# Kernel optimization log

Measured on AMD Instinct MI355X. Metric: run time of the kernel, lower is better.

## Reference

```python
import jax, jax.numpy as jnp
import numpy as np

BETA = 0.99
EPS_V = 1e-3
LOG_2PI = float(np.log(2.0 * np.pi))


def setup_inputs() -> dict:
    key = jax.random.key(0)
    ks = jax.random.split(key, 8)
    B, D, H, OUT = 2_097_152, 2, 64, 4  # OUT = 2*2*k (mu + log-var), k=1
    x = jax.random.normal(ks[0], (B, D), dtype=jnp.float32)
    y = jax.random.normal(ks[1], (B, 1, 2), dtype=jnp.float32)
    eps = jax.random.normal(ks[2], (B, 1, 2), dtype=jnp.float32)  # rsample noise
    # small init scale keeps exp(var-head) numerically tame, as trained nets would be
    W1 = 0.5 * jax.random.normal(ks[3], (D, H), dtype=jnp.float32)
    b1 = jnp.zeros((H,), dtype=jnp.float32)
    W2 = 0.1 * jax.random.normal(ks[4], (H, OUT), dtype=jnp.float32)
    b2 = jnp.zeros((OUT,), dtype=jnp.float32)
    Wv = jax.random.normal(ks[5], (D, D), dtype=jnp.float32)
    return {"x": x, "y": y, "eps": eps, "W1": W1, "b1": b1, "W2": W2, "b2": b2, "Wv": Wv}


def _V(z, Wv):
    # positive-definite Lyapunov surrogate: ||z Wv||^2 + eps, keepdims on last axis
    return jnp.sum(jnp.square(z @ Wv), axis=-1, keepdims=True) + EPS_V


def reference(x, y, eps, W1, b1, W2, b2, Wv):
    # fhat: 2 -> 64 -> 4 MLP
    fhatx = jax.nn.relu(x @ W1 + b1) @ W2 + b2            # [B, 4]
    mu = fhatx[..., :2].reshape(-1, 1, 2)                  # [B, 1, 2]
    var = jnp.exp(fhatx[..., 2:]).reshape(-1, 1, 2)        # [B, 1, 2]
    Vx = _V(x, Wv).reshape(-1, 1, 1)                       # [B, 1, 1]
    Vmu = _V(mu, Wv)                                       # [B, 1, 1]
    scale = (BETA * Vx - jax.nn.relu(BETA * Vx - Vmu)) / Vmu
    mu_stable = mu * scale                                 # [B, 1, 2]
    # diagonal-Gaussian rsample (equivalent to MVN with diag_embed(var))
    fx = mu_stable + jnp.sqrt(var) * eps                   # [B, 1, 2]
    # closed-form diagonal MVN log_prob, event dim = 2
    diff = y - mu_stable
    logp = -0.5 * (jnp.sum(diff * diff / var + jnp.log(var), axis=-1) + 2.0 * LOG_2PI)  # [B, 1]
    logp_y = -jnp.sum(logp)
    return fx, logp_y
```

## Files before the change

### kernel.cpp

```cpp
#include <hip/hip_runtime.h>
#include <math.h>


typedef float v2f __attribute__((ext_vector_type(2)));

#define GRID 1024
#define BLOCK 256
#define NPAIR 4
#define LOG_2PI 1.8378770664093453f

__device__ __forceinline__ float rcp_fast(float v) { return __builtin_amdgcn_rcpf(v); }
__device__ __forceinline__ v2f splat(float s) { v2f r; r.x = s; r.y = s; return r; }

__launch_bounds__(BLOCK, 4)
__global__ void mdn_kernel(const float* __restrict__ x,
                           const float* __restrict__ y,
                           const float* __restrict__ eps,
                           const float* __restrict__ W1,
                           const float* __restrict__ b1,
                           const float* __restrict__ W2,
                           const float* __restrict__ b2,
                           const float* __restrict__ Wv,
                           float* __restrict__ fx_out,
                           float* __restrict__ block_part,
                           int n_pairs)
{
    __shared__ float s_part[BLOCK / 64];

    const int t = threadIdx.x;
    const int T = GRID * BLOCK;
    const int g = blockIdx.x * BLOCK + t;

    const float b2_0 = b2[0], b2_1 = b2[1], b2_2 = b2[2], b2_3 = b2[3];
    const float wv00 = Wv[0], wv01 = Wv[1], wv10 = Wv[2], wv11 = Wv[3];

    float4 yv[NPAIR], ev[NPAIR];
    v2f X0[NPAIR], X1[NPAIR];
    v2f A0[NPAIR], A1[NPAIR], A2[NPAIR], A3[NPAIR];

    #pragma unroll
    for (int p = 0; p < NPAIR; ++p) {
        const int rp = g + p * T;
        float4 xv = make_float4(0.f, 0.f, 0.f, 0.f);
        yv[p] = make_float4(0.f, 0.f, 0.f, 0.f);
        ev[p] = make_float4(0.f, 0.f, 0.f, 0.f);
        if (rp < n_pairs) {
            xv    = reinterpret_cast<const float4*>(x)[rp];
            yv[p] = reinterpret_cast<const float4*>(y)[rp];
            ev[p] = reinterpret_cast<const float4*>(eps)[rp];
        }
        X0[p].x = xv.x; X0[p].y = xv.z;
        X1[p].x = xv.y; X1[p].y = xv.w;
        A0[p] = splat(b2_0); A1[p] = splat(b2_1);
        A2[p] = splat(b2_2); A3[p] = splat(b2_3);
    }

    #pragma unroll 2
    for (int c = 0; c < 16; ++c) {
        const float4 wa = *reinterpret_cast<const float4*>(W1 + 4 * c);
        const float4 wb = *reinterpret_cast<const float4*>(W1 + 64 + 4 * c);
        const float4 bb = *reinterpret_cast<const float4*>(b1 + 4 * c);
        const float4 w2r[4] = {
            reinterpret_cast<const float4*>(W2)[4 * c + 0],
            reinterpret_cast<const float4*>(W2)[4 * c + 1],
            reinterpret_cast<const float4*>(W2)[4 * c + 2],
            reinterpret_cast<const float4*>(W2)[4 * c + 3],
        };
        #pragma unroll
        for (int j = 0; j < 4; ++j) {
            const v2f waj = splat((&wa.x)[j]);
            const v2f wbj = splat((&wb.x)[j]);
            const v2f bj  = splat((&bb.x)[j]);
            const v2f w20 = splat(w2r[j].x);
            const v2f w21 = splat(w2r[j].y);
            const v2f w22 = splat(w2r[j].z);
            const v2f w23 = splat(w2r[j].w);
            #pragma unroll
            for (int p = 0; p < NPAIR; ++p) {
                v2f h = __builtin_elementwise_fma(X1[p], wbj, bj);
                h = __builtin_elementwise_fma(X0[p], waj, h);
                h = __builtin_elementwise_max(h, splat(0.f));
                A0[p] = __builtin_elementwise_fma(h, w20, A0[p]);
                A1[p] = __builtin_elementwise_fma(h, w21, A1[p]);
                A2[p] = __builtin_elementwise_fma(h, w22, A2[p]);
                A3[p] = __builtin_elementwise_fma(h, w23, A3[p]);
            }
        }
    }

    float lsum = 0.f;
    #pragma unroll
    for (int p = 0; p < NPAIR; ++p) {
        const int rp = g + p * T;
        float4 fxv;
        #pragma unroll
        for (int hh = 0; hh < 2; ++hh) {
            const float mu0 = hh ? A0[p].y : A0[p].x;
            const float mu1 = hh ? A1[p].y : A1[p].x;
            const float lv0 = hh ? A2[p].y : A2[p].x;
            const float lv1 = hh ? A3[p].y : A3[p].x;
            const float xx0 = hh ? X0[p].y : X0[p].x;
            const float xx1 = hh ? X1[p].y : X1[p].x;
            const float y0 = hh ? yv[p].z : yv[p].x;
            const float y1 = hh ? yv[p].w : yv[p].y;
            const float e0 = hh ? ev[p].z : ev[p].x;
            const float e1 = hh ? ev[p].w : ev[p].y;
            const float zx0 = fmaf(xx0, wv00, xx1 * wv10);
            const float zx1 = fmaf(xx0, wv01, xx1 * wv11);
            const float Vx  = fmaf(zx0, zx0, fmaf(zx1, zx1, 1e-3f));
            const float zm0 = fmaf(mu0, wv00, mu1 * wv10);
            const float zm1 = fmaf(mu0, wv01, mu1 * wv11);
            const float Vmu = fmaf(zm0, zm0, fmaf(zm1, zm1, 1e-3f));
            const float scale = fminf(0.99f * Vx, Vmu) * rcp_fast(Vmu);
            const float ms0 = mu0 * scale, ms1 = mu1 * scale;
            const float f0 = fmaf(__expf(0.5f * lv0), e0, ms0);
            const float f1 = fmaf(__expf(0.5f * lv1), e1, ms1);
            if (hh) { fxv.z = f0; fxv.w = f1; }
            else    { fxv.x = f0; fxv.y = f1; }
            const float d0 = y0 - ms0;
            const float d1 = y1 - ms1;
            const float q = fmaf(d0 * d0, __expf(-lv0), d1 * d1 * __expf(-lv1));
            lsum += fmaf(0.5f, q + lv0 + lv1, LOG_2PI);
        }
        if (rp < n_pairs) reinterpret_cast<float4*>(fx_out)[rp] = fxv;
    }

    #pragma unroll
    for (int off = 32; off; off >>= 1) lsum += __shfl_xor(lsum, off, 64);
    if ((t & 63) == 0) s_part[t >> 6] = lsum;
    __syncthreads();
    if (t == 0) {
        float bs = 0.f;
        #pragma unroll
        for (int w = 0; w < BLOCK / 64; ++w) bs += s_part[w];
        block_part[blockIdx.x] = bs;
    }
}

__launch_bounds__(BLOCK, 1)
__global__ void mdn_reduce_kernel(const float* __restrict__ block_part,
                                  float* __restrict__ logp_out)
{
    __shared__ float s_part[BLOCK / 64];
    const int t = threadIdx.x;
    float s = 0.f;
    #pragma unroll
    for (int k = 0; k < GRID / BLOCK; ++k) s += block_part[t + k * BLOCK];
    #pragma unroll
    for (int off = 32; off; off >>= 1) s += __shfl_xor(s, off, 64);
    if ((t & 63) == 0) s_part[t >> 6] = s;
    __syncthreads();
    if (t == 0) {
        float bs = 0.f;
        #pragma unroll
        for (int w = 0; w < BLOCK / 64; ++w) bs += s_part[w];
        *logp_out = bs;
    }
}

extern "C" void kernel_launch(void* const* d_in, const int* in_sizes, int n_in,
                              void* d_out, int out_size, void* d_ws, size_t ws_size,
                              hipStream_t stream) {
    const float* x   = (const float*)d_in[0];
    const float* y   = (const float*)d_in[1];
    const float* eps = (const float*)d_in[2];
    const float* W1  = (const float*)d_in[3];
    const float* b1  = (const float*)d_in[4];
    const float* W2  = (const float*)d_in[5];
    const float* b2  = (const float*)d_in[6];
    const float* Wv  = (const float*)d_in[7];

    const int B = in_sizes[0] / 2;
    const int n_pairs = B / 2;
    float* fx_out     = (float*)d_out;
    float* logp_out   = fx_out + (size_t)2 * B;
    float* block_part = (float*)d_ws;

    mdn_kernel<<<GRID, BLOCK, 0, stream>>>(x, y, eps, W1, b1, W2, b2, Wv,
                                           fx_out, block_part, n_pairs);
    mdn_reduce_kernel<<<1, BLOCK, 0, stream>>>(block_part, logp_out);
}
```

Baseline: 121.1 us.

## Defer y/eps loads into MLP loop and vectorize epilogue with packed math

```diff
diff --git a/kernel.cpp b/kernel.cpp
--- a/kernel.cpp
+++ b/kernel.cpp
@@ -11,6 +11,45 @@
 
 __device__ __forceinline__ float rcp_fast(float v) { return __builtin_amdgcn_rcpf(v); }
 __device__ __forceinline__ v2f splat(float s) { v2f r; r.x = s; r.y = s; return r; }
+
+__device__ __forceinline__ void mlp_chunk(int c,
+                                          const float* __restrict__ W1,
+                                          const float* __restrict__ b1,
+                                          const float* __restrict__ W2,
+                                          const v2f (&X0)[NPAIR], const v2f (&X1)[NPAIR],
+                                          v2f (&A0)[NPAIR], v2f (&A1)[NPAIR],
+                                          v2f (&A2)[NPAIR], v2f (&A3)[NPAIR])
+{
+    const float4 wa = *reinterpret_cast<const float4*>(W1 + 4 * c);
+    const float4 wb = *reinterpret_cast<const float4*>(W1 + 64 + 4 * c);
+    const float4 bb = *reinterpret_cast<const float4*>(b1 + 4 * c);
+    const float4 w2r[4] = {
+        reinterpret_cast<const float4*>(W2)[4 * c + 0],
+        reinterpret_cast<const float4*>(W2)[4 * c + 1],
+        reinterpret_cast<const float4*>(W2)[4 * c + 2],
+        reinterpret_cast<const float4*>(W2)[4 * c + 3],
+    };
+    #pragma unroll
+    for (int j = 0; j < 4; ++j) {
+        const v2f waj = splat((&wa.x)[j]);
+        const v2f wbj = splat((&wb.x)[j]);
+        const v2f bj  = splat((&bb.x)[j]);
+        const v2f w20 = splat(w2r[j].x);
+        const v2f w21 = splat(w2r[j].y);
+        const v2f w22 = splat(w2r[j].z);
+        const v2f w23 = splat(w2r[j].w);
+        #pragma unroll
+        for (int p = 0; p < NPAIR; ++p) {
+            v2f h = __builtin_elementwise_fma(X1[p], wbj, bj);
+            h = __builtin_elementwise_fma(X0[p], waj, h);
+            h = __builtin_elementwise_max(h, splat(0.f));
+            A0[p] = __builtin_elementwise_fma(h, w20, A0[p]);
+            A1[p] = __builtin_elementwise_fma(h, w21, A1[p]);
+            A2[p] = __builtin_elementwise_fma(h, w22, A2[p]);
+            A3[p] = __builtin_elementwise_fma(h, w23, A3[p]);
+        }
+    }
+}
 
 __launch_bounds__(BLOCK, 4)
 __global__ void mdn_kernel(const float* __restrict__ x,
@@ -34,100 +73,88 @@
     const float b2_0 = b2[0], b2_1 = b2[1], b2_2 = b2[2], b2_3 = b2[3];
     const float wv00 = Wv[0], wv01 = Wv[1], wv10 = Wv[2], wv11 = Wv[3];
 
-    float4 yv[NPAIR], ev[NPAIR];
-    v2f X0[NPAIR], X1[NPAIR];
+    v2f X0[NPAIR], X1[NPAIR], Vx[NPAIR];
     v2f A0[NPAIR], A1[NPAIR], A2[NPAIR], A3[NPAIR];
 
     #pragma unroll
     for (int p = 0; p < NPAIR; ++p) {
         const int rp = g + p * T;
         float4 xv = make_float4(0.f, 0.f, 0.f, 0.f);
-        yv[p] = make_float4(0.f, 0.f, 0.f, 0.f);
-        ev[p] = make_float4(0.f, 0.f, 0.f, 0.f);
-        if (rp < n_pairs) {
-            xv    = reinterpret_cast<const float4*>(x)[rp];
-            yv[p] = reinterpret_cast<const float4*>(y)[rp];
-            ev[p] = reinterpret_cast<const float4*>(eps)[rp];
-        }
+        if (rp < n_pairs) xv = reinterpret_cast<const float4*>(x)[rp];
         X0[p].x = xv.x; X0[p].y = xv.z;
         X1[p].x = xv.y; X1[p].y = xv.w;
         A0[p] = splat(b2_0); A1[p] = splat(b2_1);
         A2[p] = splat(b2_2); A3[p] = splat(b2_3);
     }
+    #pragma unroll
+    for (int p = 0; p < NPAIR; ++p) {
+        const v2f zx0 = __builtin_elementwise_fma(X0[p], splat(wv00), X1[p] * splat(wv10));
+        const v2f zx1 = __builtin_elementwise_fma(X0[p], splat(wv01), X1[p] * splat(wv11));
+        Vx[p] = __builtin_elementwise_fma(zx0, zx0,
+                __builtin_elementwise_fma(zx1, zx1, splat(1e-3f)));
+    }
 
     #pragma unroll 2
-    for (int c = 0; c < 16; ++c) {
-        const float4 wa = *reinterpret_cast<const float4*>(W1 + 4 * c);
-        const float4 wb = *reinterpret_cast<const float4*>(W1 + 64 + 4 * c);
-        const float4 bb = *reinterpret_cast<const float4*>(b1 + 4 * c);
-        const float4 w2r[4] = {
-            reinterpret_cast<const float4*>(W2)[4 * c + 0],
-            reinterpret_cast<const float4*>(W2)[4 * c + 1],
-            reinterpret_cast<const float4*>(W2)[4 * c + 2],
-            reinterpret_cast<const float4*>(W2)[4 * c + 3],
-        };
-        #pragma unroll
-        for (int j = 0; j < 4; ++j) {
-            const v2f waj = splat((&wa.x)[j]);
-            const v2f wbj = splat((&wb.x)[j]);
-            const v2f bj  = splat((&bb.x)[j]);
-            const v2f w20 = splat(w2r[j].x);
-            const v2f w21 = splat(w2r[j].y);
-            const v2f w22 = splat(w2r[j].z);
-            const v2f w23 = splat(w2r[j].w);
-            #pragma unroll
-            for (int p = 0; p < NPAIR; ++p) {
-                v2f h = __builtin_elementwise_fma(X1[p], wbj, bj);
-                h = __builtin_elementwise_fma(X0[p], waj, h);
-                h = __builtin_elementwise_max(h, splat(0.f));
-                A0[p] = __builtin_elementwise_fma(h, w20, A0[p]);
-                A1[p] = __builtin_elementwise_fma(h, w21, A1[p]);
-                A2[p] = __builtin_elementwise_fma(h, w22, A2[p]);
-                A3[p] = __builtin_elementwise_fma(h, w23, A3[p]);
-            }
+    for (int c = 0; c < 12; ++c)
+        mlp_chunk(c, W1, b1, W2, X0, X1, A0, A1, A2, A3);
+
+    float4 yv[NPAIR], ev[NPAIR];
+    #pragma unroll
+    for (int p = 0; p < NPAIR; ++p) {
+        const int rp = g + p * T;
+        yv[p] = make_float4(0.f, 0.f, 0.f, 0.f);
+        ev[p] = make_float4(0.f, 0.f, 0.f, 0.f);
+        if (rp < n_pairs) {
+            yv[p] = reinterpret_cast<const float4*>(y)[rp];
+            ev[p] = reinterpret_cast<const float4*>(eps)[rp];
         }
     }
 
-    float lsum = 0.f;
+    #pragma unroll 2
+    for (int c = 12; c < 16; ++c)
+        mlp_chunk(c, W1, b1, W2, X0, X1, A0, A1, A2, A3);
+
+    v2f lsum = splat(0.f);
     #pragma unroll
     for (int p = 0; p < NPAIR; ++p) {
         const int rp = g + p * T;
-        float4 fxv;
-        #pragma unroll
-        for (int hh = 0; hh < 2; ++hh) {
-            const float mu0 = hh ? A0[p].y : A0[p].x;
-            const float mu1 = hh ? A1[p].y : A1[p].x;
-            const float lv0 = hh ? A2[p].y : A2[p].x;
-            const float lv1 = hh ? A3[p].y : A3[p].x;
-            const float xx0 = hh ? X0[p].y : X0[p].x;
-            const float xx1 = hh ? X1[p].y : X1[p].x;
-            const float y0 = hh ? yv[p].z : yv[p].x;
-            const float y1 = hh ? yv[p].w : yv[p].y;
-            const float e0 = hh ? ev[p].z : ev[p].x;
-            const float e1 = hh ? ev[p].w : ev[p].y;
-            const float zx0 = fmaf(xx0, wv00, xx1 * wv10);
-            const float zx1 = fmaf(xx0, wv01, xx1 * wv11);
-            const float Vx  = fmaf(zx0, zx0, fmaf(zx1, zx1, 1e-3f));
-            const float zm0 = fmaf(mu0, wv00, mu1 * wv10);
-            const float zm1 = fmaf(mu0, wv01, mu1 * wv11);
-            const float Vmu = fmaf(zm0, zm0, fmaf(zm1, zm1, 1e-3f));
-            const float scale = fminf(0.99f * Vx, Vmu) * rcp_fast(Vmu);
-            const float ms0 = mu0 * scale, ms1 = mu1 * scale;
-            const float f0 = fmaf(__expf(0.5f * lv0), e0, ms0);
-            const float f1 = fmaf(__expf(0.5f * lv1), e1, ms1);
-            if (hh) { fxv.z = f0; fxv.w = f1; }
-            else    { fxv.x = f0; fxv.y = f1; }
-            const float d0 = y0 - ms0;
-            const float d1 = y1 - ms1;
-            const float q = fmaf(d0 * d0, __expf(-lv0), d1 * d1 * __expf(-lv1));
-            lsum += fmaf(0.5f, q + lv0 + lv1, LOG_2PI);
+        const v2f mu0 = A0[p], mu1 = A1[p], lv0 = A2[p], lv1 = A3[p];
+        const v2f zm0 = __builtin_elementwise_fma(mu0, splat(wv00), mu1 * splat(wv10));
+        const v2f zm1 = __builtin_elementwise_fma(mu0, splat(wv01), mu1 * splat(wv11));
+        const v2f Vmu = __builtin_elementwise_fma(zm0, zm0,
+                        __builtin_elementwise_fma(zm1, zm1, splat(1e-3f)));
+        const v2f num = __builtin_elementwise_min(splat(0.99f) * Vx[p], Vmu);
+        v2f scale;
+        scale.x = num.x * rcp_fast(Vmu.x);
+        scale.y = num.y * rcp_fast(Vmu.y);
+        const v2f ms0 = mu0 * scale, ms1 = mu1 * scale;
+        v2f sd0, sd1, iv0, iv1;
+        sd0.x = __expf(0.5f * lv0.x); sd0.y = __expf(0.5f * lv0.y);
+        sd1.x = __expf(0.5f * lv1.x); sd1.y = __expf(0.5f * lv1.y);
+        iv0.x = __expf(-lv0.x);       iv0.y = __expf(-lv0.y);
+        iv1.x = __expf(-lv1.x);       iv1.y = __expf(-lv1.y);
+        v2f e0; e0.x = ev[p].x; e0.y = ev[p].z;
+        v2f e1; e1.x = ev[p].y; e1.y = ev[p].w;
+        const v2f f0 = __builtin_elementwise_fma(sd0, e0, ms0);
+        const v2f f1 = __builtin_elementwise_fma(sd1, e1, ms1);
+        v2f y0; y0.x = yv[p].x; y0.y = yv[p].z;
+        v2f y1; y1.x = yv[p].y; y1.y = yv[p].w;
+        const v2f d0 = y0 - ms0, d1 = y1 - ms1;
+        const v2f q = __builtin_elementwise_fma(d0 * d0, iv0, (d1 * d1) * iv1);
+        if (rp < n_pairs) {
+            float4 fxv;
+            fxv.x = f0.x; fxv.y = f1.x;
+            fxv.z = f0.y; fxv.w = f1.y;
+            reinterpret_cast<float4*>(fx_out)[rp] = fxv;
+            lsum = lsum + __builtin_elementwise_fma(splat(0.5f), q + lv0 + lv1,
+                                                    splat(LOG_2PI));
         }
-        if (rp < n_pairs) reinterpret_cast<float4*>(fx_out)[rp] = fxv;
-    }
-
-    #pragma unroll
-    for (int off = 32; off; off >>= 1) lsum += __shfl_xor(lsum, off, 64);
-    if ((t & 63) == 0) s_part[t >> 6] = lsum;
+    }
+    float ls = lsum.x + lsum.y;
+
+    #pragma unroll
+    for (int off = 32; off; off >>= 1) ls += __shfl_xor(ls, off, 64);
+    if ((t & 63) == 0) s_part[t >> 6] = ls;
     __syncthreads();
     if (t == 0) {
         float bs = 0.f;
```

New measurement: 117.8 us. -2.7%, faster.
